# Optimization experiments

Measured on AMD Instinct MI355X. Metric: run time of the kernel, lower is better.

## Reference

```python
import jax, jax.numpy as jnp
import numpy as np

D = 1024
H = 16
FF = 4096
B = 2
L = 2048
EPS = 1e-5


def setup_inputs() -> dict:
    key = jax.random.key(0)
    ks = jax.random.split(key, 12)
    s = 0.02
    return {
        "x": jax.random.normal(ks[0], (B, L, D), dtype=jnp.float32),
        "ln1_g": jnp.ones((D,), jnp.float32),
        "ln1_b": jnp.zeros((D,), jnp.float32),
        "qkv_w": jax.random.normal(ks[1], (D, 3 * D), dtype=jnp.float32) * s,
        "proj_w": jax.random.normal(ks[2], (D, D), dtype=jnp.float32) * s,
        "proj_b": jnp.zeros((D,), jnp.float32),
        "ln2_g": jnp.ones((D,), jnp.float32),
        "ln2_b": jnp.zeros((D,), jnp.float32),
        "w1": jax.random.normal(ks[3], (D, FF), dtype=jnp.float32) * s,
        "b1": jnp.zeros((FF,), jnp.float32),
        "w2": jax.random.normal(ks[4], (FF, D), dtype=jnp.float32) * s,
        "b2": jnp.zeros((D,), jnp.float32),
    }


def _layernorm(x, g, b):
    mu = jnp.mean(x, axis=-1, keepdims=True)
    var = jnp.var(x, axis=-1, keepdims=True)
    return (x - mu) * jax.lax.rsqrt(var + EPS) * g + b


def _attn(x, qkv_w, proj_w, proj_b):
    Bv, Lv, Dv = x.shape
    dk = Dv // H
    qkv = x @ qkv_w  # [B,L,3D]
    q, k, v = jnp.split(qkv, 3, axis=-1)

    def split(t):
        return t.reshape(Bv, Lv, H, dk).transpose(0, 2, 1, 3)  # [B,H,L,dk]

    q, k, v = map(split, (q, k, v))
    scores = jnp.einsum("bhqd,bhkd->bhqk", q, k) / np.sqrt(dk)
    attn = jax.nn.softmax(scores, axis=-1)
    out = jnp.einsum("bhqk,bhkd->bhqd", attn, v)
    out = out.transpose(0, 2, 1, 3).reshape(Bv, Lv, Dv)
    return out @ proj_w + proj_b


def reference(x, ln1_g, ln1_b, qkv_w, proj_w, proj_b, ln2_g, ln2_b, w1, b1, w2, b2):
    x = x + _attn(_layernorm(x, ln1_g, ln1_b), qkv_w, proj_w, proj_b)
    h = _layernorm(x, ln2_g, ln2_b)
    h = jax.nn.gelu(h @ w1 + b1, approximate=False) @ w2 + b2
    return x + h
```

## Files before the change

kernel.cpp:

```cpp
#include <hip/hip_runtime.h>
#include <cstdint>
#include <cstddef>

typedef __attribute__((ext_vector_type(8))) short bf16x8;
typedef __attribute__((ext_vector_type(4))) short bf16x4;
typedef __attribute__((ext_vector_type(4))) float f32x4;

__device__ __forceinline__ uint16_t f2bf(float f) {
    uint32_t u = __float_as_uint(f);
    u += 0x7FFFu + ((u >> 16) & 1u);
    return (uint16_t)(u >> 16);
}
__device__ __forceinline__ uint32_t bfr(float f) {
    return (__float_as_uint(f) + 0x8000u) >> 16;
}

__device__ __forceinline__ f32x4 mfma16(bf16x8 a, bf16x8 b, f32x4 c) {
    return __builtin_amdgcn_mfma_f32_16x16x32_bf16(a, b, c, 0, 0, 0);
}

__device__ __forceinline__ void async_copy16(const void* g, void* l) {
    __builtin_amdgcn_global_load_lds(
        (__attribute__((address_space(1))) void*)g,
        (__attribute__((address_space(3))) void*)l, 16, 0, 0);
}

template <int N> __device__ __forceinline__ void waitvm() {
    if constexpr (N == 0) asm volatile("s_waitcnt vmcnt(0)" ::: "memory");
    else if constexpr (N == 4) asm volatile("s_waitcnt vmcnt(4)" ::: "memory");
    else if constexpr (N == 8) asm volatile("s_waitcnt vmcnt(8)" ::: "memory");
}
__device__ __forceinline__ void fence_sched() {
    asm volatile("" ::: "memory");
    __builtin_amdgcn_sched_barrier(0);
}

typedef __attribute__((address_space(3))) const uint16_t lds_cu16;
__device__ __forceinline__ bf16x4 tr_read(lds_cu16* p) {
    bf16x4 d;
    asm volatile("ds_read_b64_tr_b16 %0, %1" : "=v"(d) : "v"(p));
    return d;
}
__device__ __forceinline__ bf16x8 cat8(bf16x4 lo, bf16x4 hi) {
    return __builtin_shufflevector(lo, hi, 0, 1, 2, 3, 4, 5, 6, 7);
}

__global__ __launch_bounds__(256) void transpose_cast(const float* __restrict__ W,
                                                      uint16_t* __restrict__ Wt,
                                                      int K, int N) {
    __shared__ uint16_t tile[32][33];
    const int n0 = blockIdx.x * 32, k0 = blockIdx.y * 32;
    const int tx = threadIdx.x, ty = threadIdx.y;
#pragma unroll
    for (int j = 0; j < 4; ++j) {
        int k = k0 + ty + j * 8;
        tile[ty + j * 8][tx] = f2bf(W[(size_t)k * N + n0 + tx]);
    }
    __syncthreads();
#pragma unroll
    for (int j = 0; j < 4; ++j) {
        int n = n0 + ty + j * 8;
        Wt[(size_t)n * K + k0 + tx] = tile[tx][ty + j * 8];
    }
}

__global__ __launch_bounds__(256) void ln_kernel(const float* __restrict__ x,
                                                 const float* __restrict__ g,
                                                 const float* __restrict__ b,
                                                 uint16_t* __restrict__ out) {
    const int row = blockIdx.x;
    const int t = threadIdx.x;
    const float* xr = x + (size_t)row * 1024;
    float4 v = *(const float4*)(xr + t * 4);
    float s = v.x + v.y + v.z + v.w;
    float s2 = v.x * v.x + v.y * v.y + v.z * v.z + v.w * v.w;
#pragma unroll
    for (int off = 1; off < 64; off <<= 1) {
        s += __shfl_xor(s, off);
        s2 += __shfl_xor(s2, off);
    }
    __shared__ float sh[8];
    const int wv = t >> 6;
    if ((t & 63) == 0) { sh[wv] = s; sh[4 + wv] = s2; }
    __syncthreads();
    s = sh[0] + sh[1] + sh[2] + sh[3];
    s2 = sh[4] + sh[5] + sh[6] + sh[7];
    const float mu = s * (1.f / 1024.f);
    const float var = s2 * (1.f / 1024.f) - mu * mu;
    const float rs = rsqrtf(var + 1e-5f);
    float4 gg = *(const float4*)(g + t * 4);
    float4 bb = *(const float4*)(b + t * 4);
    ushort4 ov;
    ov.x = f2bf((v.x - mu) * rs * gg.x + bb.x);
    ov.y = f2bf((v.y - mu) * rs * gg.y + bb.y);
    ov.z = f2bf((v.z - mu) * rs * gg.z + bb.z);
    ov.w = f2bf((v.w - mu) * rs * gg.w + bb.w);
    *(ushort4*)(out + (size_t)row * 1024 + t * 4) = ov;
}

template <int EPI>
__global__ __launch_bounds__(256, 2) void gemm_kh(const uint16_t* __restrict__ A,
                                                  const uint16_t* __restrict__ Bt,
                                                  const float* __restrict__ bias,
                                                  const float* __restrict__ resid,
                                                  void* __restrict__ outp,
                                                  int M, int N, int K) {
    __shared__ uint16_t As[2][2][128][32];
    __shared__ uint16_t Bs[2][2][128][32];
    const int t = threadIdx.x, lane = t & 63, w = t >> 6;
    const int l16 = lane & 15, lhi = lane >> 4;
    const int wr = w >> 1, wc = w & 1;
    const int m0 = blockIdx.x * 128, n0 = blockIdx.y * 128;

    f32x4 acc[4][4];
    const f32x4 z = {0.f, 0.f, 0.f, 0.f};
#pragma unroll
    for (int mi = 0; mi < 4; ++mi)
#pragma unroll
        for (int ni = 0; ni < 4; ++ni) acc[mi][ni] = z;

    const int srow = w * 16 + (lane >> 2);
    const int sg = lane & 3;
    const uint16_t* Abase = A + (size_t)m0 * K;
    const uint16_t* Bbase = Bt + (size_t)n0 * K;

    auto stageH = [&](int ti, int b, int sh) {
        const int kt = ti * 64 + sh * 32;
#pragma unroll
        for (int j = 0; j < 2; ++j) {
            int r = j * 64 + srow;
            int gs = (sg ^ ((r >> 1) & 3)) << 3;
            async_copy16(Abase + (size_t)r * K + kt + gs, &As[b][sh][j * 64 + w * 16][0]);
        }
#pragma unroll
        for (int j = 0; j < 2; ++j) {
            int r = j * 64 + srow;
            int gs = (sg ^ ((r >> 1) & 3)) << 3;
            async_copy16(Bbase + (size_t)r * K + kt + gs, &Bs[b][sh][j * 64 + w * 16][0]);
        }
    };

    auto phase = [&](int p, int kh) {
        bf16x8 af[4], bfr[4];
#pragma unroll
        for (int mi = 0; mi < 4; ++mi) {
            int rr = wr * 64 + mi * 16 + l16;
            af[mi] = *(const bf16x8*)&As[p][kh][rr][(lhi ^ ((rr >> 1) & 3)) << 3];
        }
#pragma unroll
        for (int ni = 0; ni < 4; ++ni) {
            int rr = wc * 64 + ni * 16 + l16;
            bfr[ni] = *(const bf16x8*)&Bs[p][kh][rr][(lhi ^ ((rr >> 1) & 3)) << 3];
        }
        __builtin_amdgcn_s_setprio(1);
#pragma unroll
        for (int mi = 0; mi < 4; ++mi)
#pragma unroll
            for (int ni = 0; ni < 4; ++ni)
                acc[mi][ni] = mfma16(af[mi], bfr[ni], acc[mi][ni]);
        __builtin_amdgcn_s_setprio(0);
    };

    const int nt = K / 64;
    stageH(0, 0, 0);
    stageH(0, 0, 1);
    waitvm<4>();
    __builtin_amdgcn_s_barrier();
    fence_sched();

    for (int ti = 0; ti < nt; ++ti) {
        const int p = ti & 1, q = p ^ 1;
        const bool last = (ti == nt - 1);
        if (!last) stageH(ti + 1, q, 0);
        phase(p, 0);
        if (!last) stageH(ti + 1, q, 1);
        if (!last) waitvm<8>(); else waitvm<0>();
        __builtin_amdgcn_s_barrier();
        fence_sched();
        phase(p, 1);
        if (!last) {
            waitvm<4>();
            __builtin_amdgcn_s_barrier();
            fence_sched();
        }
    }

#pragma unroll
    for (int mi = 0; mi < 4; ++mi) {
#pragma unroll
        for (int ni = 0; ni < 4; ++ni) {
#pragma unroll
            for (int e = 0; e < 4; ++e) {
                int gm = m0 + wr * 64 + mi * 16 + 4 * lhi + e;
                int gn = n0 + wc * 64 + ni * 16 + l16;
                float v = acc[mi][ni][e];
                if constexpr (EPI == 0) {
                    ((uint16_t*)outp)[(size_t)gm * N + gn] = f2bf(v);
                } else if constexpr (EPI == 1) {
                    v += bias[gn] + resid[(size_t)gm * N + gn];
                    ((float*)outp)[(size_t)gm * N + gn] = v;
                } else {
                    v += bias[gn];
                    float gl = 0.5f * v * (1.f + erff(v * 0.70710678118f));
                    ((uint16_t*)outp)[(size_t)gm * N + gn] = f2bf(gl);
                }
            }
        }
    }
}

__global__ __launch_bounds__(256) void attn_kernel(const uint16_t* __restrict__ qkv,
                                                   uint16_t* __restrict__ aout) {
    __shared__ uint16_t Kt[2][64 * 64];
    __shared__ uint16_t Vs[2][64 * 64];
    __shared__ uint16_t Pq[4][16 * 64];
    const int qt = blockIdx.x, h = blockIdx.y, b = blockIdx.z;
    const int t = threadIdx.x, lane = t & 63, w = t >> 6;
    const int l16 = lane & 15, lhi = lane >> 4;
    const int q0 = qt * 64;
    const uint16_t* base = qkv + (size_t)(b * 2048) * 3072 + h * 64;

    bf16x8 aq[2];
    {
        const uint16_t* qp = base + (size_t)(q0 + w * 16 + l16) * 3072;
        aq[0] = *(const bf16x8*)(qp + 8 * lhi);
        aq[1] = *(const bf16x8*)(qp + 32 + 8 * lhi);
    }

    const int krow = lane >> 3;
    const int kgs = ((lane & 7) ^ krow) << 3;
    const int vkk = ((lane >> 5) << 2) | ((lane >> 1) & 3);
    const int vd  = (((lane >> 3) & 3) << 4) | ((lane & 1) << 3);

    auto stage = [&](int tile, int bufi) {
        const uint16_t* kb = base + (size_t)(tile * 64) * 3072 + 1024;
        const uint16_t* vb = base + (size_t)(tile * 64) * 3072 + 2048;
#pragma unroll
        for (int p = 0; p < 2; ++p) {
            int r0 = w * 16 + p * 8;
            async_copy16(kb + (size_t)(r0 + krow) * 3072 + kgs, &Kt[bufi][r0 * 64]);
        }
#pragma unroll
        for (int p = 0; p < 2; ++p) {
            int i = w * 2 + p;
            async_copy16(vb + (size_t)(i * 8 + vkk) * 3072 + vd, &Vs[bufi][i * 512]);
        }
    };

    const f32x4 z = {0.f, 0.f, 0.f, 0.f};
    f32x4 oaccT[4];
#pragma unroll
    for (int n = 0; n < 4; ++n) oaccT[n] = z;
    float lrun = 0.f;
    const float cs = 0.18033688f;

    stage(0, 0);
    __syncthreads();

    for (int tile = 0; tile < 32; ++tile) {
        const int cur = tile & 1;
        if (tile + 1 < 32) stage(tile + 1, cur ^ 1);

        f32x4 sacc[4];
#pragma unroll
        for (int nk = 0; nk < 4; ++nk) sacc[nk] = z;
#pragma unroll
        for (int nk = 0; nk < 4; ++nk) {
#pragma unroll
            for (int kh = 0; kh < 2; ++kh) {
                const int gk = kh * 4 + lhi;
                const int rr = nk * 16 + l16;
                bf16x8 bk = *(const bf16x8*)&Kt[cur][rr * 64 + ((gk ^ (l16 & 7)) << 3)];
                sacc[nk] = mfma16(bk, aq[kh], sacc[nk]);
            }
        }

        float p[4][4];
        float ps = 0.f;
#pragma unroll
        for (int nk = 0; nk < 4; ++nk)
#pragma unroll
            for (int e = 0; e < 4; ++e) {
                float pe = exp2f(sacc[nk][e] * cs);
                p[nk][e] = pe;
                ps += pe;
            }
        ps += __shfl_xor(ps, 16);
        ps += __shfl_xor(ps, 32);
        lrun += ps;

#pragma unroll
        for (int nk = 0; nk < 4; ++nk) {
            uint2 pk;
            pk.x = bfr(p[nk][0]) | (bfr(p[nk][1]) << 16);
            pk.y = bfr(p[nk][2]) | (bfr(p[nk][3]) << 16);
            const int g = nk * 2 + (lhi >> 1);
            *(uint2*)&Pq[w][l16 * 64 + ((g ^ (l16 & 7)) << 3) + ((lhi & 1) << 2)] = pk;
        }
        asm volatile("s_waitcnt lgkmcnt(0)" ::: "memory");
        __builtin_amdgcn_sched_barrier(0);

        bf16x8 pa[2];
#pragma unroll
        for (int kh = 0; kh < 2; ++kh) {
            const int gk = kh * 4 + lhi;
            pa[kh] = *(const bf16x8*)&Pq[w][l16 * 64 + ((gk ^ (l16 & 7)) << 3)];
        }
        lds_cu16* vtb = (lds_cu16*)&Vs[cur][0];
        bf16x8 bv[4][2];
#pragma unroll
        for (int n = 0; n < 4; ++n) {
#pragma unroll
            for (int kh = 0; kh < 2; ++kh) {
                const int gk = kh * 4 + lhi;
                bf16x4 lo = tr_read(vtb + ((gk * 2) << 8) + (n << 6) + l16);
                bf16x4 hi = tr_read(vtb + ((gk * 2 + 1) << 8) + (n << 6) + l16);
                bv[n][kh] = cat8(lo, hi);
            }
        }
        asm volatile("s_waitcnt lgkmcnt(0)" ::: "memory");
        __builtin_amdgcn_sched_barrier(0);

#pragma unroll
        for (int n = 0; n < 4; ++n)
#pragma unroll
            for (int kh = 0; kh < 2; ++kh)
                oaccT[n] = mfma16(bv[n][kh], pa[kh], oaccT[n]);

        __syncthreads();
    }

    const float rl = 1.0f / lrun;
    const size_t orow = (size_t)(b * 2048 + q0 + w * 16 + l16) * 1024 + h * 64;
#pragma unroll
    for (int n = 0; n < 4; ++n) {
        ushort4 ov;
        ov.x = f2bf(oaccT[n][0] * rl);
        ov.y = f2bf(oaccT[n][1] * rl);
        ov.z = f2bf(oaccT[n][2] * rl);
        ov.w = f2bf(oaccT[n][3] * rl);
        *(ushort4*)&aout[orow + n * 16 + 4 * lhi] = ov;
    }
}

extern "C" void kernel_launch(void* const* d_in, const int* in_sizes, int n_in,
                              void* d_out, int out_size, void* d_ws, size_t ws_size,
                              hipStream_t stream) {
    const float* x      = (const float*)d_in[0];
    const float* ln1_g  = (const float*)d_in[1];
    const float* ln1_b  = (const float*)d_in[2];
    const float* qkv_w  = (const float*)d_in[3];
    const float* proj_w = (const float*)d_in[4];
    const float* proj_b = (const float*)d_in[5];
    const float* ln2_g  = (const float*)d_in[6];
    const float* ln2_b  = (const float*)d_in[7];
    const float* w1     = (const float*)d_in[8];
    const float* b1     = (const float*)d_in[9];
    const float* w2     = (const float*)d_in[10];
    const float* b2     = (const float*)d_in[11];
    float* out = (float*)d_out;

    char* ws = (char*)d_ws;
    size_t off = 0;
    auto alloc = [&](size_t bytes) {
        void* p = ws + off;
        off += (bytes + 255) & ~(size_t)255;
        return p;
    };
    uint16_t* wqkv_t  = (uint16_t*)alloc((size_t)3072 * 1024 * 2);
    uint16_t* wproj_t = (uint16_t*)alloc((size_t)1024 * 1024 * 2);
    uint16_t* w1_t    = (uint16_t*)alloc((size_t)4096 * 1024 * 2);
    uint16_t* w2_t    = (uint16_t*)alloc((size_t)1024 * 4096 * 2);
    float*    x2      = (float*)   alloc((size_t)4096 * 1024 * 4);
    uint16_t* lnb     = (uint16_t*)alloc((size_t)4096 * 1024 * 2);
    uint16_t* qkvb    = (uint16_t*)alloc((size_t)4096 * 3072 * 2);
    uint16_t* attnb   = (uint16_t*)alloc((size_t)4096 * 1024 * 2);
    uint16_t* h1      = qkvb;

    dim3 tb(32, 8, 1);
    transpose_cast<<<dim3(3072 / 32, 1024 / 32), tb, 0, stream>>>(qkv_w, wqkv_t, 1024, 3072);
    transpose_cast<<<dim3(1024 / 32, 1024 / 32), tb, 0, stream>>>(proj_w, wproj_t, 1024, 1024);
    transpose_cast<<<dim3(4096 / 32, 1024 / 32), tb, 0, stream>>>(w1, w1_t, 1024, 4096);
    transpose_cast<<<dim3(1024 / 32, 4096 / 32), tb, 0, stream>>>(w2, w2_t, 4096, 1024);

    ln_kernel<<<4096, 256, 0, stream>>>(x, ln1_g, ln1_b, lnb);
    gemm_kh<0><<<dim3(32, 24), 256, 0, stream>>>(lnb, wqkv_t, nullptr, nullptr, qkvb, 4096, 3072, 1024);
    attn_kernel<<<dim3(32, 16, 2), 256, 0, stream>>>(qkvb, attnb);
    gemm_kh<1><<<dim3(32, 8), 256, 0, stream>>>(attnb, wproj_t, proj_b, x, x2, 4096, 1024, 1024);
    ln_kernel<<<4096, 256, 0, stream>>>(x2, ln2_g, ln2_b, lnb);
    gemm_kh<2><<<dim3(32, 32), 256, 0, stream>>>(lnb, w1_t, b1, nullptr, h1, 4096, 4096, 1024);
    gemm_kh<1><<<dim3(32, 8), 256, 0, stream>>>(h1, w2_t, b2, x2, out, 4096, 1024, 4096);
}
```

Before: 299.5 us.

## Add 256x256 GEMM tile for wide GEMMs and split-K the narrow GEMMs

Adds a 512-thread GEMM kernel with 256x256 output tiles and an XOR-swizzled LDS layout, used for the QKV and FF1 projections to raise data reuse per block. The narrow N=1024 GEMMs (attention projection and FF2) are split into two K-halves launched back to back; the second launch accumulates into the fp32 output with read-modify-write. The large tiles leave only 192 and 256 blocks for those GEMMs, which risks poor CU occupancy. Split-K runs as two serial launches that re-read and re-write the output, so it adds traffic without adding parallelism.

```diff
diff --git a/kernel.cpp b/kernel.cpp
--- a/kernel.cpp
+++ b/kernel.cpp
@@ -27,6 +27,7 @@
 
 template <int N> __device__ __forceinline__ void waitvm() {
     if constexpr (N == 0) asm volatile("s_waitcnt vmcnt(0)" ::: "memory");
+    else if constexpr (N == 2) asm volatile("s_waitcnt vmcnt(2)" ::: "memory");
     else if constexpr (N == 4) asm volatile("s_waitcnt vmcnt(4)" ::: "memory");
     else if constexpr (N == 8) asm volatile("s_waitcnt vmcnt(8)" ::: "memory");
 }
@@ -99,12 +100,125 @@
 }
 
 template <int EPI>
+__global__ __launch_bounds__(512, 2) void gemm256(const uint16_t* __restrict__ A,
+                                                  const uint16_t* __restrict__ Bt,
+                                                  const float* __restrict__ bias,
+                                                  const float* __restrict__ resid,
+                                                  void* __restrict__ outp,
+                                                  int M, int N, int K) {
+    __shared__ uint16_t As[2][2][256 * 32];
+    __shared__ uint16_t Bs[2][2][256 * 32];
+    const int t = threadIdx.x, lane = t & 63, w = t >> 6;
+    const int l16 = lane & 15, lhi = lane >> 4;
+    const int wm = w >> 2, wn = w & 3;
+    const int m0 = blockIdx.x * 256, n0 = blockIdx.y * 256;
+
+    f32x4 acc[8][4];
+    const f32x4 z = {0.f, 0.f, 0.f, 0.f};
+#pragma unroll
+    for (int mi = 0; mi < 8; ++mi)
+#pragma unroll
+        for (int ni = 0; ni < 4; ++ni) acc[mi][ni] = z;
+
+    const int strow = t >> 2;
+    const int stlg = (t & 3) ^ ((t >> 2) & 3) ^ ((t >> 4) & 3);
+    const uint16_t* Ab = A + (size_t)m0 * K;
+    const uint16_t* Bb = Bt + (size_t)n0 * K;
+    const int keyL = (l16 & 3) ^ ((l16 >> 2) & 3);
+    const int rgr = (lhi ^ keyL) * 8;
+
+    auto stA = [&](int ti, int b, int kh) {
+#pragma unroll
+        for (int j = 0; j < 2; ++j) {
+            int row = j * 128 + strow;
+            async_copy16(Ab + (size_t)row * K + ti * 64 + kh * 32 + stlg * 8,
+                         &As[b][kh][(j * 128 + w * 16) * 32]);
+        }
+    };
+    auto stB = [&](int ti, int b, int kh) {
+#pragma unroll
+        for (int j = 0; j < 2; ++j) {
+            int row = j * 128 + strow;
+            async_copy16(Bb + (size_t)row * K + ti * 64 + kh * 32 + stlg * 8,
+                         &Bs[b][kh][(j * 128 + w * 16) * 32]);
+        }
+    };
+
+    auto phase = [&](int p, int kh) {
+        bf16x8 af[8], bf[4];
+#pragma unroll
+        for (int mi = 0; mi < 8; ++mi)
+            af[mi] = *(const bf16x8*)&As[p][kh][(wm * 128 + mi * 16 + l16) * 32 + rgr];
+#pragma unroll
+        for (int ni = 0; ni < 4; ++ni)
+            bf[ni] = *(const bf16x8*)&Bs[p][kh][(wn * 64 + ni * 16 + l16) * 32 + rgr];
+        __builtin_amdgcn_s_setprio(1);
+#pragma unroll
+        for (int mi = 0; mi < 8; ++mi)
+#pragma unroll
+            for (int ni = 0; ni < 4; ++ni)
+                acc[mi][ni] = mfma16(af[mi], bf[ni], acc[mi][ni]);
+        __builtin_amdgcn_s_setprio(0);
+    };
+
+    const int nt = K / 64;
+    stB(0, 0, 0); stB(0, 0, 1); stA(0, 0, 0); stA(0, 0, 1);
+    waitvm<2>();
+    __builtin_amdgcn_s_barrier();
+    fence_sched();
+
+    for (int ti = 0; ti < nt; ++ti) {
+        const int p = ti & 1, q = p ^ 1;
+        const bool last = (ti == nt - 1);
+        if (!last) { stB(ti + 1, q, 0); stB(ti + 1, q, 1); }
+        phase(p, 0);
+        if (last) waitvm<0>(); else waitvm<4>();
+        __builtin_amdgcn_s_barrier();
+        fence_sched();
+        if (!last) { stA(ti + 1, q, 0); stA(ti + 1, q, 1); }
+        phase(p, 1);
+        if (!last) {
+            waitvm<2>();
+            __builtin_amdgcn_s_barrier();
+            fence_sched();
+        }
+    }
+
+#pragma unroll
+    for (int mi = 0; mi < 8; ++mi) {
+#pragma unroll
+        for (int ni = 0; ni < 4; ++ni) {
+#pragma unroll
+            for (int e = 0; e < 4; ++e) {
+                int gm = m0 + wm * 128 + mi * 16 + 4 * lhi + e;
+                int gn = n0 + wn * 64 + ni * 16 + l16;
+                float v = acc[mi][ni][e];
+                if constexpr (EPI == 0) {
+                    ((uint16_t*)outp)[(size_t)gm * N + gn] = f2bf(v);
+                } else if constexpr (EPI == 1) {
+                    v += bias[gn] + resid[(size_t)gm * N + gn];
+                    ((float*)outp)[(size_t)gm * N + gn] = v;
+                } else if constexpr (EPI == 2) {
+                    v += bias[gn];
+                    float gl = 0.5f * v * (1.f + erff(v * 0.70710678118f));
+                    ((uint16_t*)outp)[(size_t)gm * N + gn] = f2bf(gl);
+                } else {
+                    float* o = (float*)outp;
+                    o[(size_t)gm * N + gn] += v;
+                }
+            }
+        }
+    }
+}
+
+template <int EPI>
 __global__ __launch_bounds__(256, 2) void gemm_kh(const uint16_t* __restrict__ A,
                                                   const uint16_t* __restrict__ Bt,
                                                   const float* __restrict__ bias,
                                                   const float* __restrict__ resid,
                                                   void* __restrict__ outp,
-                                                  int M, int N, int K) {
+                                                  int M, int N, int K,
+                                                  int k0, int kext) {
     __shared__ uint16_t As[2][2][128][32];
     __shared__ uint16_t Bs[2][2][128][32];
     const int t = threadIdx.x, lane = t & 63, w = t >> 6;
@@ -161,16 +275,16 @@
         __builtin_amdgcn_s_setprio(0);
     };
 
-    const int nt = K / 64;
-    stageH(0, 0, 0);
-    stageH(0, 0, 1);
+    const int t0 = k0 / 64, t1 = (k0 + kext) / 64;
+    stageH(t0, 0, 0);
+    stageH(t0, 0, 1);
     waitvm<4>();
     __builtin_amdgcn_s_barrier();
     fence_sched();
 
-    for (int ti = 0; ti < nt; ++ti) {
-        const int p = ti & 1, q = p ^ 1;
-        const bool last = (ti == nt - 1);
+    for (int ti = t0; ti < t1; ++ti) {
+        const int p = (ti - t0) & 1, q = p ^ 1;
+        const bool last = (ti == t1 - 1);
         if (!last) stageH(ti + 1, q, 0);
         phase(p, 0);
         if (!last) stageH(ti + 1, q, 1);
@@ -194,15 +308,12 @@
                 int gm = m0 + wr * 64 + mi * 16 + 4 * lhi + e;
                 int gn = n0 + wc * 64 + ni * 16 + l16;
                 float v = acc[mi][ni][e];
-                if constexpr (EPI == 0) {
-                    ((uint16_t*)outp)[(size_t)gm * N + gn] = f2bf(v);
-                } else if constexpr (EPI == 1) {
+                if constexpr (EPI == 1) {
                     v += bias[gn] + resid[(size_t)gm * N + gn];
                     ((float*)outp)[(size_t)gm * N + gn] = v;
                 } else {
-                    v += bias[gn];
-                    float gl = 0.5f * v * (1.f + erff(v * 0.70710678118f));
-                    ((uint16_t*)outp)[(size_t)gm * N + gn] = f2bf(gl);
+                    float* o = (float*)outp;
+                    o[(size_t)gm * N + gn] += v;
                 }
             }
         }
@@ -384,10 +495,12 @@
     transpose_cast<<<dim3(1024 / 32, 4096 / 32), tb, 0, stream>>>(w2, w2_t, 4096, 1024);
 
     ln_kernel<<<4096, 256, 0, stream>>>(x, ln1_g, ln1_b, lnb);
-    gemm_kh<0><<<dim3(32, 24), 256, 0, stream>>>(lnb, wqkv_t, nullptr, nullptr, qkvb, 4096, 3072, 1024);
+    gemm256<0><<<dim3(16, 12), 512, 0, stream>>>(lnb, wqkv_t, nullptr, nullptr, qkvb, 4096, 3072, 1024);
     attn_kernel<<<dim3(32, 16, 2), 256, 0, stream>>>(qkvb, attnb);
-    gemm_kh<1><<<dim3(32, 8), 256, 0, stream>>>(attnb, wproj_t, proj_b, x, x2, 4096, 1024, 1024);
+    gemm_kh<1><<<dim3(32, 8), 256, 0, stream>>>(attnb, wproj_t, proj_b, x, x2, 4096, 1024, 1024, 0, 512);
+    gemm_kh<3><<<dim3(32, 8), 256, 0, stream>>>(attnb, wproj_t, nullptr, nullptr, x2, 4096, 1024, 1024, 512, 512);
     ln_kernel<<<4096, 256, 0, stream>>>(x2, ln2_g, ln2_b, lnb);
-    gemm_kh<2><<<dim3(32, 32), 256, 0, stream>>>(lnb, w1_t, b1, nullptr, h1, 4096, 4096, 1024);
-    gemm_kh<1><<<dim3(32, 8), 256, 0, stream>>>(h1, w2_t, b2, x2, out, 4096, 1024, 4096);
-}
+    gemm256<2><<<dim3(16, 16), 512, 0, stream>>>(lnb, w1_t, b1, nullptr, h1, 4096, 4096, 1024);
+    gemm_kh<1><<<dim3(32, 8), 256, 0, stream>>>(h1, w2_t, b2, x2, out, 4096, 1024, 4096, 0, 2048);
+    gemm_kh<3><<<dim3(32, 8), 256, 0, stream>>>(h1, w2_t, nullptr, nullptr, out, 4096, 1024, 4096, 2048, 2048);
+}
```

Result: slower. 354.0 us (+18.2%).

## Add XCD-aware block swizzle and split-K into two sequential launches for N=1024 GEMMs

Applied to the files above, without the earlier changes.

Remaps workgroup IDs so that consecutive tiles land on the same XCD, improving L2 reuse in the GEMMs and the attention kernel. The projection and FFN-down GEMMs are split along K into two sequential launches. The second launch uses a new epilogue that adds its partial sum into the fp32 output. Each launch still has only 256 workgroups, so occupancy does not rise. The split mainly adds an extra read-modify-write of the output and an extra launch, with no parallelism gained.

```diff
diff --git a/kernel.cpp b/kernel.cpp
--- a/kernel.cpp
+++ b/kernel.cpp
@@ -43,6 +43,10 @@
 }
 __device__ __forceinline__ bf16x8 cat8(bf16x4 lo, bf16x4 hi) {
     return __builtin_shufflevector(lo, hi, 0, 1, 2, 3, 4, 5, 6, 7);
+}
+
+__device__ __forceinline__ int xcd_swz(int lin, int nwg) {
+    return (lin & 7) * (nwg >> 3) + (lin >> 3);
 }
 
 __global__ __launch_bounds__(256) void transpose_cast(const float* __restrict__ W,
@@ -104,13 +108,16 @@
                                                   const float* __restrict__ bias,
                                                   const float* __restrict__ resid,
                                                   void* __restrict__ outp,
-                                                  int M, int N, int K) {
+                                                  int M, int N, int K,
+                                                  int k0, int kext) {
     __shared__ uint16_t As[2][2][128][32];
     __shared__ uint16_t Bs[2][2][128][32];
     const int t = threadIdx.x, lane = t & 63, w = t >> 6;
     const int l16 = lane & 15, lhi = lane >> 4;
     const int wr = w >> 1, wc = w & 1;
-    const int m0 = blockIdx.x * 128, n0 = blockIdx.y * 128;
+    const int nwg = gridDim.x * gridDim.y;
+    const int sl = xcd_swz(blockIdx.y * gridDim.x + blockIdx.x, nwg);
+    const int m0 = (sl % gridDim.x) * 128, n0 = (sl / gridDim.x) * 128;
 
     f32x4 acc[4][4];
     const f32x4 z = {0.f, 0.f, 0.f, 0.f};
@@ -161,16 +168,16 @@
         __builtin_amdgcn_s_setprio(0);
     };
 
-    const int nt = K / 64;
-    stageH(0, 0, 0);
-    stageH(0, 0, 1);
+    const int t0 = k0 / 64, t1 = (k0 + kext) / 64;
+    stageH(t0, 0, 0);
+    stageH(t0, 0, 1);
     waitvm<4>();
     __builtin_amdgcn_s_barrier();
     fence_sched();
 
-    for (int ti = 0; ti < nt; ++ti) {
-        const int p = ti & 1, q = p ^ 1;
-        const bool last = (ti == nt - 1);
+    for (int ti = t0; ti < t1; ++ti) {
+        const int p = (ti - t0) & 1, q = p ^ 1;
+        const bool last = (ti == t1 - 1);
         if (!last) stageH(ti + 1, q, 0);
         phase(p, 0);
         if (!last) stageH(ti + 1, q, 1);
@@ -199,10 +206,13 @@
                 } else if constexpr (EPI == 1) {
                     v += bias[gn] + resid[(size_t)gm * N + gn];
                     ((float*)outp)[(size_t)gm * N + gn] = v;
-                } else {
+                } else if constexpr (EPI == 2) {
                     v += bias[gn];
                     float gl = 0.5f * v * (1.f + erff(v * 0.70710678118f));
                     ((uint16_t*)outp)[(size_t)gm * N + gn] = f2bf(gl);
+                } else {
+                    float* o = (float*)outp;
+                    o[(size_t)gm * N + gn] += v;
                 }
             }
         }
@@ -214,7 +224,9 @@
     __shared__ uint16_t Kt[2][64 * 64];
     __shared__ uint16_t Vs[2][64 * 64];
     __shared__ uint16_t Pq[4][16 * 64];
-    const int qt = blockIdx.x, h = blockIdx.y, b = blockIdx.z;
+    const int lin = (blockIdx.z * gridDim.y + blockIdx.y) * gridDim.x + blockIdx.x;
+    const int sl = xcd_swz(lin, gridDim.x * gridDim.y * gridDim.z);
+    const int qt = sl & 31, h = (sl >> 5) & 15, b = sl >> 9;
     const int t = threadIdx.x, lane = t & 63, w = t >> 6;
     const int l16 = lane & 15, lhi = lane >> 4;
     const int q0 = qt * 64;
@@ -384,10 +396,12 @@
     transpose_cast<<<dim3(1024 / 32, 4096 / 32), tb, 0, stream>>>(w2, w2_t, 4096, 1024);
 
     ln_kernel<<<4096, 256, 0, stream>>>(x, ln1_g, ln1_b, lnb);
-    gemm_kh<0><<<dim3(32, 24), 256, 0, stream>>>(lnb, wqkv_t, nullptr, nullptr, qkvb, 4096, 3072, 1024);
+    gemm_kh<0><<<dim3(32, 24), 256, 0, stream>>>(lnb, wqkv_t, nullptr, nullptr, qkvb, 4096, 3072, 1024, 0, 1024);
     attn_kernel<<<dim3(32, 16, 2), 256, 0, stream>>>(qkvb, attnb);
-    gemm_kh<1><<<dim3(32, 8), 256, 0, stream>>>(attnb, wproj_t, proj_b, x, x2, 4096, 1024, 1024);
+    gemm_kh<1><<<dim3(32, 8), 256, 0, stream>>>(attnb, wproj_t, proj_b, x, x2, 4096, 1024, 1024, 0, 512);
+    gemm_kh<3><<<dim3(32, 8), 256, 0, stream>>>(attnb, wproj_t, nullptr, nullptr, x2, 4096, 1024, 1024, 512, 512);
     ln_kernel<<<4096, 256, 0, stream>>>(x2, ln2_g, ln2_b, lnb);
-    gemm_kh<2><<<dim3(32, 32), 256, 0, stream>>>(lnb, w1_t, b1, nullptr, h1, 4096, 4096, 1024);
-    gemm_kh<1><<<dim3(32, 8), 256, 0, stream>>>(h1, w2_t, b2, x2, out, 4096, 1024, 4096);
-}
+    gemm_kh<2><<<dim3(32, 32), 256, 0, stream>>>(lnb, w1_t, b1, nullptr, h1, 4096, 4096, 1024, 0, 1024);
+    gemm_kh<1><<<dim3(32, 8), 256, 0, stream>>>(h1, w2_t, b2, x2, out, 4096, 1024, 4096, 0, 2048);
+    gemm_kh<3><<<dim3(32, 8), 256, 0, stream>>>(h1, w2_t, nullptr, nullptr, out, 4096, 1024, 4096, 2048, 2048);
+}
```

Result: slower. 345.4 us (+15.3%).
